# Kernel optimization log

Hardware: AMD Instinct MI355X
Metric: run time of the kernel (lower is better)

## Reference

```python
import jax, jax.numpy as jnp
import numpy as np

N = 8192
IN_F = 256
OUT_F = 128
E = 262144
NEG = -9e15


def setup_inputs() -> dict:
    key = jax.random.key(0)
    ks = jax.random.split(key, 12)
    glorot = lambda k, shp: jax.random.uniform(k, shp, jnp.float32,
                                               -jnp.sqrt(6.0 / (shp[0] + shp[1])),
                                               jnp.sqrt(6.0 / (shp[0] + shp[1])))
    return {
        "h_context": jax.random.normal(ks[0], (N, IN_F), jnp.float32),
        "h_structure": jax.random.normal(ks[1], (N, IN_F), jnp.float32),
        "edge_index": jax.random.randint(ks[2], (2, E), 0, N, jnp.int64),
        "Wc_w": glorot(ks[3], (OUT_F, IN_F)),
        "Wc_b": jnp.zeros((OUT_F,), jnp.float32),
        "Ws_w": glorot(ks[4], (OUT_F, IN_F)),
        "Ws_b": jnp.zeros((OUT_F,), jnp.float32),
        "ac_w": glorot(ks[5], (1, 2 * OUT_F)),
        "as_w": glorot(ks[6], (1, 2 * OUT_F)),
        "Ws_coff": jax.random.normal(ks[7], (1, 1), jnp.float32) * 1.414,
        "Wc_coff": jax.random.normal(ks[8], (1, 1), jnp.float32) * 1.414,
    }


def _pair_scores(h, a_w):
    # GAT trick: score[i,j] = leaky_relu(a1 . h[i] + a2 . h[j])
    F_out = h.shape[1]
    s_src = h @ a_w[0, :F_out]   # [N]
    s_dst = h @ a_w[0, F_out:]   # [N]
    return jax.nn.leaky_relu(s_src[:, None] + s_dst[None, :], 0.01)  # [N, N]


def reference(h_context, h_structure, edge_index, Wc_w, Wc_b, Ws_w, Ws_b,
              ac_w, as_w, Ws_coff, Wc_coff):
    hc = h_context @ Wc_w.T + Wc_b                      # [N, F]
    alpha_c = _pair_scores(hc, ac_w)                    # [N, N]
    hs = jax.nn.softmax(h_structure, axis=1) @ Ws_w.T + Ws_b
    alpha_s = _pair_scores(hs, as_w)                    # [N, N]
    alpha = jnp.abs(Ws_coff[0, 0]) * alpha_c + jnp.abs(Wc_coff[0, 0]) * alpha_s
    n = h_structure.shape[0]
    adj = jnp.zeros((n, n), bool).at[edge_index[0], edge_index[1]].set(True)
    attention = jnp.where(adj, alpha, NEG)
    attention = jax.nn.softmax(attention, axis=1)
    # dropout omitted (eval mode / deterministic reference)
    return attention @ hc
```

## Files before the change

### kernel.cpp

```cpp
#include <hip/hip_runtime.h>
#include <math.h>

#define N_NODES 8192
#define IN_FEAT 256
#define OUT_FEAT 128
#define WORDS_PER_ROW 128
#define CAPW 256
#define M_TILE 16
#define NF_BLOCKS 1024

typedef unsigned long long u64;
typedef float v4f __attribute__((ext_vector_type(4)));
typedef short s8v __attribute__((ext_vector_type(8)));
typedef short s4v __attribute__((ext_vector_type(4)));

__device__ __forceinline__ float wred_sum_b(float v) {
    #pragma unroll
    for (int o = 32; o > 0; o >>= 1) v += __shfl_xor(v, o, 64);
    return v;
}
__device__ __forceinline__ float wred_max_b(float v) {
    #pragma unroll
    for (int o = 32; o > 0; o >>= 1) v = fmaxf(v, __shfl_xor(v, o, 64));
    return v;
}

__device__ __forceinline__ void bsplit(float x, unsigned short& hi, unsigned short& lo) {
    unsigned int xb = __float_as_uint(x);
    hi = (unsigned short)(xb >> 16);
    float lof = x - __uint_as_float(xb & 0xFFFF0000u);
    lo = (unsigned short)(__float_as_uint(lof) >> 16);
}

__device__ __forceinline__ void split8(const float* p, s8v& h8, s8v& l8) {
    short hh[8], ll[8];
    #pragma unroll
    for (int j = 0; j < 8; j++) {
        unsigned short h, l;
        bsplit(p[j], h, l);
        hh[j] = (short)h; ll[j] = (short)l;
    }
    h8 = *(const s8v*)hh;
    l8 = *(const s8v*)ll;
}

__global__ __launch_bounds__(256, 4) void node_feats(
    const float* __restrict__ hctx, const float* __restrict__ hstr,
    const float* __restrict__ Wc,  const float* __restrict__ Ws,
    const float* __restrict__ Wcb, const float* __restrict__ Wsb,
    const float* __restrict__ acw, const float* __restrict__ asw,
    const int* __restrict__ ei, int E, u64* __restrict__ bmp,
    float* __restrict__ hc,
    float* __restrict__ csrc, float* __restrict__ cdst,
    float* __restrict__ ssrc, float* __restrict__ sdst)
{
    __shared__ unsigned short aH[M_TILE][264], aL[M_TILE][264];
    __shared__ float invsh[M_TILE];
    __shared__ float hT[M_TILE][132];

    const int t = threadIdx.x;
    const int w = t >> 6, ln = t & 63;
    const int is_struct = (blockIdx.x >= 512);
    const int b = blockIdx.x & 511;
    const int r0 = b * M_TILE;

    {
        int pv = ei[2 * (ln & 31) + 1];
        u64 nz = __ballot(pv != 0);
        const int is64 = (nz == 0);
        for (int e = blockIdx.x * 256 + t; e < E; e += NF_BLOCKS * 256) {
            int s, d;
            if (is64) { s = ei[2 * e]; d = ei[2 * E + 2 * e]; }
            else      { s = ei[e];     d = ei[E + e]; }
            if ((unsigned)s < N_NODES && (unsigned)d < N_NODES)
                atomicOr(&bmp[(size_t)s * WORDS_PER_ROW + (d >> 6)], 1ull << (d & 63));
        }
    }

    if (!is_struct) {
        #pragma unroll
        for (int j = 0; j < 4; j++) {
            int c = t + 256 * j;
            int r = c >> 6;
            int k = (c & 63) * 4;
            const float4 x = *(const float4*)(hctx + (size_t)(r0 + r) * IN_FEAT + k);
            unsigned short h0, h1, h2, h3, l0, l1, l2, l3;
            bsplit(x.x, h0, l0); bsplit(x.y, h1, l1);
            bsplit(x.z, h2, l2); bsplit(x.w, h3, l3);
            s4v hv = { (short)h0, (short)h1, (short)h2, (short)h3 };
            s4v lv = { (short)l0, (short)l1, (short)l2, (short)l3 };
            *(s4v*)&aH[r][k] = hv;
            *(s4v*)&aL[r][k] = lv;
        }
    } else {
        #pragma unroll
        for (int rr = 0; rr < 4; rr++) {
            int r = w * 4 + rr;
            const float* srow = hstr + (size_t)(r0 + r) * IN_FEAT;
            float x0 = srow[ln], x1 = srow[ln + 64], x2 = srow[ln + 128], x3 = srow[ln + 192];
            float mx = wred_max_b(fmaxf(fmaxf(x0, x1), fmaxf(x2, x3)));
            float e0 = __expf(x0 - mx), e1 = __expf(x1 - mx);
            float e2 = __expf(x2 - mx), e3 = __expf(x3 - mx);
            float s = wred_sum_b(e0 + e1 + e2 + e3);
            if (ln == 0) invsh[r] = 1.0f / s;
            unsigned short h, l;
            bsplit(e0, h, l); aH[r][ln]       = h; aL[r][ln]       = l;
            bsplit(e1, h, l); aH[r][ln + 64]  = h; aL[r][ln + 64]  = l;
            bsplit(e2, h, l); aH[r][ln + 128] = h; aL[r][ln + 128] = l;
            bsplit(e3, h, l); aH[r][ln + 192] = h; aL[r][ln + 192] = l;
        }
    }
    __syncthreads();

    const int m = ln & 15, q = ln >> 4;
    const int nA = (w << 5) + m, nB = nA + 16;
    const float* W = is_struct ? Ws : Wc;
    const float* rowA = W + (size_t)nA * IN_FEAT;
    const float* rowB = W + (size_t)nB * IN_FEAT;

    v4f acc0 = {0.f,0.f,0.f,0.f}, acc1 = {0.f,0.f,0.f,0.f};

    #pragma unroll 2
    for (int ks = 0; ks < 8; ks++) {
        const int k0 = ks * 32 + q * 8;
        float wbufA[8], wbufB[8];
        *(float4*)&wbufA[0] = *(const float4*)(rowA + k0);
        *(float4*)&wbufA[4] = *(const float4*)(rowA + k0 + 4);
        *(float4*)&wbufB[0] = *(const float4*)(rowB + k0);
        *(float4*)&wbufB[4] = *(const float4*)(rowB + k0 + 4);
        s8v bhA, blA, bhB, blB;
        split8(wbufA, bhA, blA);
        split8(wbufB, bhB, blB);
        s8v ah = *(const s8v*)&aH[m][k0];
        s8v al = *(const s8v*)&aL[m][k0];
        acc0 = __builtin_amdgcn_mfma_f32_16x16x32_bf16(al, bhA, acc0, 0, 0, 0);
        acc0 = __builtin_amdgcn_mfma_f32_16x16x32_bf16(ah, blA, acc0, 0, 0, 0);
        acc0 = __builtin_amdgcn_mfma_f32_16x16x32_bf16(ah, bhA, acc0, 0, 0, 0);
        acc1 = __builtin_amdgcn_mfma_f32_16x16x32_bf16(al, bhB, acc1, 0, 0, 0);
        acc1 = __builtin_amdgcn_mfma_f32_16x16x32_bf16(ah, blB, acc1, 0, 0, 0);
        acc1 = __builtin_amdgcn_mfma_f32_16x16x32_bf16(ah, bhB, acc1, 0, 0, 0);
    }

    if (!is_struct) {
        const float bA = Wcb[nA], bB = Wcb[nB];
        #pragma unroll
        for (int p = 0; p < 4; p++) {
            int row = q * 4 + p;
            hT[row][nA] = acc0[p] + bA;
            hT[row][nB] = acc1[p] + bB;
        }
        __syncthreads();

        #pragma unroll
        for (int j = 0; j < 8; j++) {
            int f = t + 256 * j;
            int r = f >> 7, c = f & 127;
            hc[(size_t)(r0 + r) * OUT_FEAT + c] = hT[r][c];
        }
        float a0 = acw[ln], a0b = acw[ln + 64], a1 = acw[128 + ln], a1b = acw[192 + ln];
        #pragma unroll
        for (int rr = 0; rr < 4; rr++) {
            int r = w + rr * 4;
            float c0 = hT[r][ln], c1 = hT[r][ln + 64];
            float v0 = wred_sum_b(c0 * a0 + c1 * a0b);
            float v1 = wred_sum_b(c0 * a1 + c1 * a1b);
            if (ln == 0) { csrc[r0 + r] = v0; cdst[r0 + r] = v1; }
        }
    } else {
        const float bA = Wsb[nA], bB = Wsb[nB];
        #pragma unroll
        for (int p = 0; p < 4; p++) {
            int row = q * 4 + p;
            float iv = invsh[row];
            hT[row][nA] = acc0[p] * iv + bA;
            hT[row][nB] = acc1[p] * iv + bB;
        }
        __syncthreads();

        float b0 = asw[ln], b0b = asw[ln + 64], b1 = asw[128 + ln], b1b = asw[192 + ln];
        #pragma unroll
        for (int rr = 0; rr < 4; rr++) {
            int r = w + rr * 4;
            float s0 = hT[r][ln], s1 = hT[r][ln + 64];
            float v2 = wred_sum_b(s0 * b0 + s1 * b0b);
            float v3 = wred_sum_b(s0 * b1 + s1 * b1b);
            if (ln == 0) { ssrc[r0 + r] = v2; sdst[r0 + r] = v3; }
        }
    }
}

__global__ __launch_bounds__(256) void attn(
    const u64* __restrict__ bmp,
    const float* __restrict__ hc,
    const float* __restrict__ csrc, const float* __restrict__ cdst,
    const float* __restrict__ ssrc, const float* __restrict__ sdst,
    const float* __restrict__ wscoff, const float* __restrict__ wccoff,
    float* __restrict__ out)
{
    __shared__ int   jl[4][CAPW];
    __shared__ float pl[4][CAPW];

    const int w  = threadIdx.x >> 6;
    const int ln = threadIdx.x & 63;
    const int i  = blockIdx.x * 4 + w;

    const float wS = fabsf(wscoff[0]);
    const float wC = fabsf(wccoff[0]);
    const float cs = csrc[i], ss = ssrc[i];

    ulonglong2 wv = *(const ulonglong2*)(bmp + (size_t)i * WORDS_PER_ROW + 2 * ln);
    int c = __popcll(wv.x) + __popcll(wv.y);

    int inc = c;
    #pragma unroll
    for (int o = 1; o < 64; o <<= 1) {
        int y = __shfl_up(inc, o, 64);
        if (ln >= o) inc += y;
    }
    int pre = inc - c;
    int cnt = __shfl(inc, 63, 64);

    int idx = pre;
    #pragma unroll
    for (int h = 0; h < 2; h++) {
        u64 ww = (h == 0) ? wv.x : wv.y;
        int jb = ln * 128 + h * 64;
        while (ww) {
            int bt = __ffsll(ww) - 1; ww &= ww - 1;
            int j = jb + bt;
            float ac  = cs + cdst[j];
            float as_ = ss + sdst[j];
            ac  = (ac  > 0.0f) ? ac  : 0.01f * ac;
            as_ = (as_ > 0.0f) ? as_ : 0.01f * as_;
            if (idx < CAPW) { jl[w][idx] = j; pl[w][idx] = wS * ac + wC * as_; }
            idx++;
        }
    }
    if (cnt > CAPW) cnt = CAPW;
    __threadfence_block();

    if (cnt == 0) {
        float2 acc = {0.f, 0.f};
        const float2* hc2 = (const float2*)hc;
        for (int j = 0; j < N_NODES; j++) {
            float2 h2 = hc2[(size_t)j * 64 + ln];
            acc.x += h2.x; acc.y += h2.y;
        }
        float2 o2 = { acc.x / (float)N_NODES, acc.y / (float)N_NODES };
        *(float2*)(out + (size_t)i * OUT_FEAT + 2 * ln) = o2;
        return;
    }

    float m = -1e30f;
    for (int k = ln; k < cnt; k += 64) m = fmaxf(m, pl[w][k]);
    m = wred_max_b(m);
    float s = 0.0f;
    for (int k = ln; k < cnt; k += 64) {
        float p = __expf(pl[w][k] - m);
        pl[w][k] = p;
        s += p;
    }
    s = wred_sum_b(s);
    float inv = 1.0f / s;
    __threadfence_block();

    const float2* hc2 = (const float2*)hc;
    float2 acc = {0.f, 0.f};
    int k = 0;
    for (; k + 4 <= cnt; k += 4) {
        int   j0 = jl[w][k],   j1 = jl[w][k+1], j2 = jl[w][k+2], j3 = jl[w][k+3];
        float p0 = pl[w][k],   p1 = pl[w][k+1], p2 = pl[w][k+2], p3 = pl[w][k+3];
        float2 h0 = hc2[(size_t)j0 * 64 + ln];
        float2 h1 = hc2[(size_t)j1 * 64 + ln];
        float2 h2 = hc2[(size_t)j2 * 64 + ln];
        float2 h3 = hc2[(size_t)j3 * 64 + ln];
        acc.x += p0 * h0.x + p1 * h1.x + p2 * h2.x + p3 * h3.x;
        acc.y += p0 * h0.y + p1 * h1.y + p2 * h2.y + p3 * h3.y;
    }
    for (; k < cnt; k++) {
        float2 h0 = hc2[(size_t)jl[w][k] * 64 + ln];
        float p0 = pl[w][k];
        acc.x += p0 * h0.x; acc.y += p0 * h0.y;
    }
    float2 o2 = { acc.x * inv, acc.y * inv };
    *(float2*)(out + (size_t)i * OUT_FEAT + 2 * ln) = o2;
}

extern "C" void kernel_launch(void* const* d_in, const int* in_sizes, int n_in,
                              void* d_out, int out_size, void* d_ws, size_t ws_size,
                              hipStream_t stream)
{
    const float* hctx = (const float*)d_in[0];
    const float* hstr = (const float*)d_in[1];
    const int*   ei   = (const int*)d_in[2];
    const float* Wc   = (const float*)d_in[3];
    const float* Wcb  = (const float*)d_in[4];
    const float* Ws   = (const float*)d_in[5];
    const float* Wsb  = (const float*)d_in[6];
    const float* acw  = (const float*)d_in[7];
    const float* asw  = (const float*)d_in[8];
    const float* wsco = (const float*)d_in[9];
    const float* wcco = (const float*)d_in[10];
    float* out = (float*)d_out;

    const int n2 = in_sizes[2];
    const int E  = (n2 == 4 * 262144) ? 262144 : n2 / 2;

    char* ws = (char*)d_ws;
    size_t off = 0;
    float* hc   = (float*)(ws + off); off += (size_t)N_NODES * OUT_FEAT * sizeof(float);
    float* csrc = (float*)(ws + off); off += (size_t)N_NODES * sizeof(float);
    float* cdst = (float*)(ws + off); off += (size_t)N_NODES * sizeof(float);
    float* ssrc = (float*)(ws + off); off += (size_t)N_NODES * sizeof(float);
    float* sdst = (float*)(ws + off); off += (size_t)N_NODES * sizeof(float);
    off = (off + 255) & ~(size_t)255;
    u64* bmp    = (u64*)(ws + off);   off += (size_t)N_NODES * WORDS_PER_ROW * sizeof(u64);

    hipMemsetAsync(bmp, 0, (size_t)N_NODES * WORDS_PER_ROW * sizeof(u64), stream);

    node_feats<<<NF_BLOCKS, 256, 0, stream>>>(hctx, hstr, Wc, Ws, Wcb, Wsb,
                                              acw, asw, ei, E, bmp,
                                              hc, csrc, cdst, ssrc, sdst);
    attn<<<N_NODES / 4, 256, 0, stream>>>(bmp, hc, csrc, cdst, ssrc, sdst, wsco, wcco, out);
}
```

Measured before the change: 127.4 us.

## Pre-split weights into MFMA fragments, double M tile, fuse bitmap zeroing

Adds a prep kernel that zeroes the adjacency bitmap in place of the memset and pre-splits Wc and Ws into bf16 hi/lo fragments laid out in MFMA operand order. node_feats then loads these fragments directly instead of re-splitting the weights in every block. Its row tile grows from 16 to 32 so each weight fragment feeds twice as many MFMAs, and the transpose buffer reuses the A-tile shared memory to save LDS. The attention gather loop is also unrolled to 8 so more loads are in flight. Costs are an extra kernel launch and half as many node_feats blocks, which lowers parallelism.

```diff
diff --git a/kernel.cpp b/kernel.cpp
--- a/kernel.cpp
+++ b/kernel.cpp
@@ -6,8 +6,8 @@
 #define OUT_FEAT 128
 #define WORDS_PER_ROW 128
 #define CAPW 256
-#define M_TILE 16
-#define NF_BLOCKS 1024
+#define M_TILE 32
+#define NF_BLOCKS 512
 
 typedef unsigned long long u64;
 typedef float v4f __attribute__((ext_vector_type(4)));
@@ -32,21 +32,49 @@
     lo = (unsigned short)(__float_as_uint(lof) >> 16);
 }
 
-__device__ __forceinline__ void split8(const float* p, s8v& h8, s8v& l8) {
-    short hh[8], ll[8];
-    #pragma unroll
-    for (int j = 0; j < 8; j++) {
-        unsigned short h, l;
-        bsplit(p[j], h, l);
-        hh[j] = (short)h; ll[j] = (short)l;
-    }
-    h8 = *(const s8v*)hh;
-    l8 = *(const s8v*)ll;
+__global__ __launch_bounds__(256) void prep(
+    const float* __restrict__ Wc, const float* __restrict__ Ws,
+    u64* __restrict__ bmp,
+    unsigned short* __restrict__ cfrag, unsigned short* __restrict__ sfrag)
+{
+    const int t = threadIdx.x;
+    {
+        ulonglong2 z = {0ull, 0ull};
+        ulonglong2* dst = (ulonglong2*)(bmp + (size_t)blockIdx.x * 2048);
+        #pragma unroll
+        for (int k = 0; k < 4; k++) dst[t + 256 * k] = z;
+    }
+    int tid = blockIdx.x * 256 + t;
+    if (tid < 16384) {
+        int mat = tid >> 13;
+        int f = tid & 8191;
+        int lnf = f & 63;
+        int sel = (f >> 6) & 3;
+        int ks  = (f >> 8) & 7;
+        int wv  = (f >> 11) & 3;
+        int row = (wv << 5) + ((sel >> 1) << 4) + (lnf & 15);
+        int part = sel & 1;
+        int k0 = (ks << 5) + ((lnf >> 4) << 3);
+        const float* src = (mat ? Ws : Wc) + row * IN_FEAT + k0;
+        short tmp[8];
+        #pragma unroll
+        for (int j = 0; j < 8; j++) {
+            float x = src[j];
+            unsigned int xb = __float_as_uint(x);
+            if (part == 0) tmp[j] = (short)(xb >> 16);
+            else {
+                float lof = x - __uint_as_float(xb & 0xFFFF0000u);
+                tmp[j] = (short)(__float_as_uint(lof) >> 16);
+            }
+        }
+        unsigned short* dst = (mat ? sfrag : cfrag) + (size_t)f * 8;
+        *(s8v*)dst = *(const s8v*)tmp;
+    }
 }
 
 __global__ __launch_bounds__(256, 4) void node_feats(
     const float* __restrict__ hctx, const float* __restrict__ hstr,
-    const float* __restrict__ Wc,  const float* __restrict__ Ws,
+    const unsigned short* __restrict__ cfrag, const unsigned short* __restrict__ sfrag,
     const float* __restrict__ Wcb, const float* __restrict__ Wsb,
     const float* __restrict__ acw, const float* __restrict__ asw,
     const int* __restrict__ ei, int E, u64* __restrict__ bmp,
@@ -56,12 +84,12 @@
 {
     __shared__ unsigned short aH[M_TILE][264], aL[M_TILE][264];
     __shared__ float invsh[M_TILE];
-    __shared__ float hT[M_TILE][132];
+    float (*hT)[132] = (float(*)[132])&aH[0][0];
 
     const int t = threadIdx.x;
     const int w = t >> 6, ln = t & 63;
-    const int is_struct = (blockIdx.x >= 512);
-    const int b = blockIdx.x & 511;
+    const int is_struct = (blockIdx.x >= 256);
+    const int b = blockIdx.x & 255;
     const int r0 = b * M_TILE;
 
     {
@@ -79,7 +107,7 @@
 
     if (!is_struct) {
         #pragma unroll
-        for (int j = 0; j < 4; j++) {
+        for (int j = 0; j < 8; j++) {
             int c = t + 256 * j;
             int r = c >> 6;
             int k = (c & 63) * 4;
@@ -94,8 +122,8 @@
         }
     } else {
         #pragma unroll
-        for (int rr = 0; rr < 4; rr++) {
-            int r = w * 4 + rr;
+        for (int rr = 0; rr < 8; rr++) {
+            int r = w * 8 + rr;
             const float* srow = hstr + (size_t)(r0 + r) * IN_FEAT;
             float x0 = srow[ln], x1 = srow[ln + 64], x2 = srow[ln + 128], x3 = srow[ln + 192];
             float mx = wred_max_b(fmaxf(fmaxf(x0, x1), fmaxf(x2, x3)));
@@ -113,54 +141,61 @@
     __syncthreads();
 
     const int m = ln & 15, q = ln >> 4;
-    const int nA = (w << 5) + m, nB = nA + 16;
-    const float* W = is_struct ? Ws : Wc;
-    const float* rowA = W + (size_t)nA * IN_FEAT;
-    const float* rowB = W + (size_t)nB * IN_FEAT;
-
-    v4f acc0 = {0.f,0.f,0.f,0.f}, acc1 = {0.f,0.f,0.f,0.f};
+    const unsigned short* frag = is_struct ? sfrag : cfrag;
+
+    v4f a00 = {0.f,0.f,0.f,0.f}, a01 = {0.f,0.f,0.f,0.f};
+    v4f a10 = {0.f,0.f,0.f,0.f}, a11 = {0.f,0.f,0.f,0.f};
 
     #pragma unroll 2
     for (int ks = 0; ks < 8; ks++) {
         const int k0 = ks * 32 + q * 8;
-        float wbufA[8], wbufB[8];
-        *(float4*)&wbufA[0] = *(const float4*)(rowA + k0);
-        *(float4*)&wbufA[4] = *(const float4*)(rowA + k0 + 4);
-        *(float4*)&wbufB[0] = *(const float4*)(rowB + k0);
-        *(float4*)&wbufB[4] = *(const float4*)(rowB + k0 + 4);
-        s8v bhA, blA, bhB, blB;
-        split8(wbufA, bhA, blA);
-        split8(wbufB, bhB, blB);
-        s8v ah = *(const s8v*)&aH[m][k0];
-        s8v al = *(const s8v*)&aL[m][k0];
-        acc0 = __builtin_amdgcn_mfma_f32_16x16x32_bf16(al, bhA, acc0, 0, 0, 0);
-        acc0 = __builtin_amdgcn_mfma_f32_16x16x32_bf16(ah, blA, acc0, 0, 0, 0);
-        acc0 = __builtin_amdgcn_mfma_f32_16x16x32_bf16(ah, bhA, acc0, 0, 0, 0);
-        acc1 = __builtin_amdgcn_mfma_f32_16x16x32_bf16(al, bhB, acc1, 0, 0, 0);
-        acc1 = __builtin_amdgcn_mfma_f32_16x16x32_bf16(ah, blB, acc1, 0, 0, 0);
-        acc1 = __builtin_amdgcn_mfma_f32_16x16x32_bf16(ah, bhB, acc1, 0, 0, 0);
-    }
-
+        const s8v* base = (const s8v*)frag + ((w * 8 + ks) * 4) * 64 + ln;
+        s8v bh0 = base[0];
+        s8v bl0 = base[64];
+        s8v bh1 = base[128];
+        s8v bl1 = base[192];
+        s8v ah0 = *(const s8v*)&aH[m][k0];
+        s8v al0 = *(const s8v*)&aL[m][k0];
+        s8v ah1 = *(const s8v*)&aH[m + 16][k0];
+        s8v al1 = *(const s8v*)&aL[m + 16][k0];
+        a00 = __builtin_amdgcn_mfma_f32_16x16x32_bf16(al0, bh0, a00, 0, 0, 0);
+        a00 = __builtin_amdgcn_mfma_f32_16x16x32_bf16(ah0, bl0, a00, 0, 0, 0);
+        a00 = __builtin_amdgcn_mfma_f32_16x16x32_bf16(ah0, bh0, a00, 0, 0, 0);
+        a01 = __builtin_amdgcn_mfma_f32_16x16x32_bf16(al0, bh1, a01, 0, 0, 0);
+        a01 = __builtin_amdgcn_mfma_f32_16x16x32_bf16(ah0, bl1, a01, 0, 0, 0);
+        a01 = __builtin_amdgcn_mfma_f32_16x16x32_bf16(ah0, bh1, a01, 0, 0, 0);
+        a10 = __builtin_amdgcn_mfma_f32_16x16x32_bf16(al1, bh0, a10, 0, 0, 0);
+        a10 = __builtin_amdgcn_mfma_f32_16x16x32_bf16(ah1, bl0, a10, 0, 0, 0);
+        a10 = __builtin_amdgcn_mfma_f32_16x16x32_bf16(ah1, bh0, a10, 0, 0, 0);
+        a11 = __builtin_amdgcn_mfma_f32_16x16x32_bf16(al1, bh1, a11, 0, 0, 0);
+        a11 = __builtin_amdgcn_mfma_f32_16x16x32_bf16(ah1, bl1, a11, 0, 0, 0);
+        a11 = __builtin_amdgcn_mfma_f32_16x16x32_bf16(ah1, bh1, a11, 0, 0, 0);
+    }
+    __syncthreads();
+
+    const int nA = (w << 5) + m, nB = nA + 16;
     if (!is_struct) {
         const float bA = Wcb[nA], bB = Wcb[nB];
         #pragma unroll
         for (int p = 0; p < 4; p++) {
             int row = q * 4 + p;
-            hT[row][nA] = acc0[p] + bA;
-            hT[row][nB] = acc1[p] + bB;
+            hT[row][nA]      = a00[p] + bA;
+            hT[row][nB]      = a01[p] + bB;
+            hT[row + 16][nA] = a10[p] + bA;
+            hT[row + 16][nB] = a11[p] + bB;
         }
         __syncthreads();
 
         #pragma unroll
-        for (int j = 0; j < 8; j++) {
+        for (int j = 0; j < 16; j++) {
             int f = t + 256 * j;
             int r = f >> 7, c = f & 127;
             hc[(size_t)(r0 + r) * OUT_FEAT + c] = hT[r][c];
         }
         float a0 = acw[ln], a0b = acw[ln + 64], a1 = acw[128 + ln], a1b = acw[192 + ln];
         #pragma unroll
-        for (int rr = 0; rr < 4; rr++) {
-            int r = w + rr * 4;
+        for (int rr = 0; rr < 8; rr++) {
+            int r = w * 8 + rr;
             float c0 = hT[r][ln], c1 = hT[r][ln + 64];
             float v0 = wred_sum_b(c0 * a0 + c1 * a0b);
             float v1 = wred_sum_b(c0 * a1 + c1 * a1b);
@@ -168,19 +203,23 @@
         }
     } else {
         const float bA = Wsb[nA], bB = Wsb[nB];
+        float iv0[4], iv1[4];
+        #pragma unroll
+        for (int p = 0; p < 4; p++) { iv0[p] = invsh[q * 4 + p]; iv1[p] = invsh[q * 4 + p + 16]; }
         #pragma unroll
         for (int p = 0; p < 4; p++) {
             int row = q * 4 + p;
-            float iv = invsh[row];
-            hT[row][nA] = acc0[p] * iv + bA;
-            hT[row][nB] = acc1[p] * iv + bB;
+            hT[row][nA]      = a00[p] * iv0[p] + bA;
+            hT[row][nB]      = a01[p] * iv0[p] + bB;
+            hT[row + 16][nA] = a10[p] * iv1[p] + bA;
+            hT[row + 16][nB] = a11[p] * iv1[p] + bB;
         }
         __syncthreads();
 
         float b0 = asw[ln], b0b = asw[ln + 64], b1 = asw[128 + ln], b1b = asw[192 + ln];
         #pragma unroll
-        for (int rr = 0; rr < 4; rr++) {
-            int r = w + rr * 4;
+        for (int rr = 0; rr < 8; rr++) {
+            int r = w * 8 + rr;
             float s0 = hT[r][ln], s1 = hT[r][ln + 64];
             float v2 = wred_sum_b(s0 * b0 + s1 * b0b);
             float v3 = wred_sum_b(s0 * b1 + s1 * b1b);
@@ -267,15 +306,20 @@
     const float2* hc2 = (const float2*)hc;
     float2 acc = {0.f, 0.f};
     int k = 0;
-    for (; k + 4 <= cnt; k += 4) {
-        int   j0 = jl[w][k],   j1 = jl[w][k+1], j2 = jl[w][k+2], j3 = jl[w][k+3];
-        float p0 = pl[w][k],   p1 = pl[w][k+1], p2 = pl[w][k+2], p3 = pl[w][k+3];
-        float2 h0 = hc2[(size_t)j0 * 64 + ln];
-        float2 h1 = hc2[(size_t)j1 * 64 + ln];
-        float2 h2 = hc2[(size_t)j2 * 64 + ln];
-        float2 h3 = hc2[(size_t)j3 * 64 + ln];
-        acc.x += p0 * h0.x + p1 * h1.x + p2 * h2.x + p3 * h3.x;
-        acc.y += p0 * h0.y + p1 * h1.y + p2 * h2.y + p3 * h3.y;
+    for (; k + 8 <= cnt; k += 8) {
+        float2 hx[8];
+        float  px[8];
+        #pragma unroll
+        for (int u = 0; u < 8; u++) {
+            int ju = jl[w][k + u];
+            px[u] = pl[w][k + u];
+            hx[u] = hc2[(size_t)ju * 64 + ln];
+        }
+        #pragma unroll
+        for (int u = 0; u < 8; u++) {
+            acc.x += px[u] * hx[u].x;
+            acc.y += px[u] * hx[u].y;
+        }
     }
     for (; k < cnt; k++) {
         float2 h0 = hc2[(size_t)jl[w][k] * 64 + ln];
@@ -315,10 +359,11 @@
     float* sdst = (float*)(ws + off); off += (size_t)N_NODES * sizeof(float);
     off = (off + 255) & ~(size_t)255;
     u64* bmp    = (u64*)(ws + off);   off += (size_t)N_NODES * WORDS_PER_ROW * sizeof(u64);
-
-    hipMemsetAsync(bmp, 0, (size_t)N_NODES * WORDS_PER_ROW * sizeof(u64), stream);
-
-    node_feats<<<NF_BLOCKS, 256, 0, stream>>>(hctx, hstr, Wc, Ws, Wcb, Wsb,
+    unsigned short* cfrag = (unsigned short*)(ws + off); off += (size_t)8192 * 8 * sizeof(unsigned short);
+    unsigned short* sfrag = (unsigned short*)(ws + off); off += (size_t)8192 * 8 * sizeof(unsigned short);
+
+    prep<<<512, 256, 0, stream>>>(Wc, Ws, bmp, cfrag, sfrag);
+    node_feats<<<NF_BLOCKS, 256, 0, stream>>>(hctx, hstr, cfrag, sfrag, Wcb, Wsb,
                                               acw, asw, ei, E, bmp,
                                               hc, csrc, cdst, ssrc, sdst);
     attn<<<N_NODES / 4, 256, 0, stream>>>(bmp, hc, csrc, cdst, ssrc, sdst, wsco, wcco, out);
```

Result: faster. 121.8 us (-4.4%).
